# Kernel tuning notes

Hardware: AMD Instinct MI355X
Metric: run time of the kernel (lower is better)

## Reference

```python
import jax, jax.numpy as jnp
import numpy as np

T, B, D, H, NQ = 512, 128, 512, 64, 64  # seq_len, batch, input_dim, hidden_dim == n_qubits
EPS = 1e-5

def setup_inputs() -> dict:
    key = jax.random.key(0)
    ks = jax.random.split(key, 11)
    s = 0.05
    return {
        "inputs": jax.random.normal(ks[0], (T, B, D), jnp.float32),
        "W0": jax.random.normal(ks[1], (4, NQ, D + H), jnp.float32) * s,
        "b0": jax.random.normal(ks[2], (4, NQ), jnp.float32) * s,
        "th0": jax.random.normal(ks[3], (4, NQ), jnp.float32) * s,
        "g0": jnp.ones((H,), jnp.float32),
        "be0": jnp.zeros((H,), jnp.float32),
        "W1": jax.random.normal(ks[4], (4, NQ, H + H), jnp.float32) * s,
        "b1": jax.random.normal(ks[5], (4, NQ), jnp.float32) * s,
        "th1": jax.random.normal(ks[6], (4, NQ), jnp.float32) * s,
        "g1": jnp.ones((H,), jnp.float32),
        "be1": jnp.zeros((H,), jnp.float32),
    }

def _qlstm_layer(x, W, b, th, gamma, beta):
    # x: [T, B, Din]. Faithful to source: h_prev = c_prev = 0 at EVERY timestep
    # (the torch code never writes back `states` inside the time loop), so all
    # timesteps are independent and fully vectorized.
    zeros_h = jnp.zeros(x.shape[:-1] + (H,), x.dtype)
    combined = jnp.concatenate([x, zeros_h], axis=-1)           # [T,B,Din+H]
    # 4 gate linears stacked on leading axis g: forget, input, update, output
    z = jnp.einsum('tbk,gnk->gtbn', combined, W) + b[:, None, None, :]
    # quantum circuit closed form: RX(z_i+th_i) per qubit + CNOT ladder + <Z_k>
    #   => cumprod_{i<=k} cos(z_i + th_i)
    q = jnp.cumprod(jnp.cos(z + th[:, None, None, :]), axis=-1)  # [4,T,B,NQ]
    sg = jax.nn.sigmoid(q)
    i_g = sg[1]
    g_g = jnp.tanh(sg[2])
    o_g = sg[3]
    # c = f * c_prev + i * g, with c_prev == 0  (f gate has no effect)
    c = i_g * g_g                                                # [T,B,H]
    h = o_g * jnp.tanh(c)
    mu = jnp.mean(h, axis=-1, keepdims=True)
    var = jnp.mean((h - mu) ** 2, axis=-1, keepdims=True)
    h_ln = (h - mu) * jax.lax.rsqrt(var + EPS) * gamma + beta
    return h_ln, c

def reference(inputs, W0, b0, th0, g0, be0, W1, b1, th1, g1, be1):
    h0, c0 = _qlstm_layer(inputs, W0, b0, th0, g0, be0)  # layer 0 (no dropout: p=0)
    h1, c1 = _qlstm_layer(h0, W1, b1, th1, g1, be1)      # layer 1
    outputs = h1                                          # [T,B,H]
    # new_states = states at the last timestep: [(h_ln, c)] per layer
    return (outputs, h0[-1], c0[-1], h1[-1], c1[-1])
```

## Files before the change

kernel.cpp:

```cpp
#include <hip/hip_runtime.h>
#include <hip/hip_bf16.h>

typedef __attribute__((ext_vector_type(8))) short bf16x8;
typedef _Float16 f16x8 __attribute__((ext_vector_type(8)));
typedef __attribute__((ext_vector_type(4))) float f32x4;

#define T_SEQ   512
#define B_BATCH 128
#define H_DIM   64
#define MB      64
#define AS_STRIDE 72
#define ZS_STRIDE 193
#define HS_STRIDE 68
#define LASTROW ((T_SEQ - 1) * B_BATCH)

#define W0HF 0
#define W0HB 98304
#define W0LB 196608
#define W1HF 294912
#define W1HB 307200
#define W1LB 319488

__device__ __forceinline__ void splitH(float f, unsigned& hf, unsigned& hb, unsigned& lb) {
    _Float16 h = (_Float16)f;
    hf = (unsigned)__builtin_bit_cast(unsigned short, h);
    float r = f - (float)h;
    hb = (unsigned)__builtin_bit_cast(unsigned short, __float2bfloat16(f));
    lb = (unsigned)__builtin_bit_cast(unsigned short, __float2bfloat16(r));
}

__device__ __forceinline__ void splitH8(const float* p, uint4& Pf, uint4& Pb, uint4& Pl) {
    float4 a = *(const float4*)p;
    float4 b = *(const float4*)(p + 4);
    float v[8] = {a.x, a.y, a.z, a.w, b.x, b.y, b.z, b.w};
    unsigned f[8], hb[8], lb[8];
#pragma unroll
    for (int i = 0; i < 8; ++i) splitH(v[i], f[i], hb[i], lb[i]);
    Pf = (uint4){f[0] | (f[1] << 16), f[2] | (f[3] << 16), f[4] | (f[5] << 16), f[6] | (f[7] << 16)};
    Pb = (uint4){hb[0] | (hb[1] << 16), hb[2] | (hb[3] << 16), hb[4] | (hb[5] << 16), hb[6] | (hb[7] << 16)};
    Pl = (uint4){lb[0] | (lb[1] << 16), lb[2] | (lb[3] << 16), lb[4] | (lb[5] << 16), lb[6] | (lb[7] << 16)};
}

__device__ __forceinline__ f32x4 mfma3(f16x8 af, bf16x8 ab, bf16x8 al,
                                       f16x8 bf, bf16x8 bb, bf16x8 bl, f32x4 c) {
    c = __builtin_amdgcn_mfma_f32_16x16x32_f16(af, bf, c, 0, 0, 0);
    c = __builtin_amdgcn_mfma_f32_16x16x32_bf16(ab, bl, c, 0, 0, 0);
    c = __builtin_amdgcn_mfma_f32_16x16x32_bf16(al, bb, c, 0, 0, 0);
    return c;
}

__device__ __forceinline__ float acc_sigmoid(float x) {
    float e = expf(-x);
    float d = 1.0f + e;
    float r = __builtin_amdgcn_rcpf(d);
    r = r * (2.0f - d * r);
    return r;
}

__device__ __forceinline__ float scan_prod(float v, int lane) {
    for (int d = 1; d < 64; d <<= 1) {
        float t = __shfl_up(v, d);
        v *= (lane >= d) ? t : 1.0f;
    }
    return v;
}

__device__ __forceinline__ float wave_sum(float v) {
    for (int d = 1; d < 64; d <<= 1) v += __shfl_xor(v, d);
    return v;
}

__global__ __launch_bounds__(256) void presplit_w(const float* __restrict__ W0,
                                                  const float* __restrict__ W1,
                                                  unsigned short* __restrict__ ws) {
    int i = blockIdx.x * 256 + threadIdx.x;
    if (i < 98304) {
        int r = i >> 9, k = i & 511;
        unsigned hf, hb, lb;
        splitH(W0[(r + 64) * 576 + k], hf, hb, lb);
        ws[W0HF + i] = (unsigned short)hf;
        ws[W0HB + i] = (unsigned short)hb;
        ws[W0LB + i] = (unsigned short)lb;
    } else if (i < 110592) {
        int j = i - 98304;
        int r = j >> 6, k = j & 63;
        unsigned hf, hb, lb;
        splitH(W1[(r + 64) * 128 + k], hf, hb, lb);
        ws[W1HF + j] = (unsigned short)hf;
        ws[W1HB + j] = (unsigned short)hb;
        ws[W1LB + j] = (unsigned short)lb;
    }
}

__global__ __launch_bounds__(256) void qlstm_fused(
    const float* __restrict__ x,
    const float* __restrict__ b0,
    const float* __restrict__ th0,
    const float* __restrict__ g0,
    const float* __restrict__ be0,
    const float* __restrict__ b1,
    const float* __restrict__ th1,
    const float* __restrict__ g1,
    const float* __restrict__ be1,
    const unsigned short* __restrict__ wsp,
    float* __restrict__ out)
{
    __shared__ __align__(16) char lds[45056];
    unsigned short* phf = (unsigned short*)lds;
    unsigned short* phb = phf + MB * AS_STRIDE;
    unsigned short* plb = phb + MB * AS_STRIDE;
    float* zs = (float*)lds;
    float* hs = (float*)(lds + 27648);

    const int tid = threadIdx.x;
    const long rowbase = (long)blockIdx.x * MB;

    float* out0 = out;
    float* out1 = out + (long)T_SEQ * B_BATCH * H_DIM;
    float* out2 = out1 + B_BATCH * H_DIM;
    float* out3 = out2 + B_BATCH * H_DIM;
    float* out4 = out3 + B_BATCH * H_DIM;

    const int lane = tid & 63;
    const int wave = tid >> 6;
    const int ln   = lane & 15;
    const int quad = lane >> 4;
    const int cw   = wave * 48;

    const float bt0a = b0[64  + lane] + th0[64  + lane];
    const float bt0b = b0[128 + lane] + th0[128 + lane];
    const float bt0c = b0[192 + lane] + th0[192 + lane];
    const float bt1a = b1[64  + lane] + th1[64  + lane];
    const float bt1b = b1[128 + lane] + th1[128 + lane];
    const float bt1c = b1[192 + lane] + th1[192 + lane];
    const float g0v = g0[lane], be0v = be0[lane];
    const float g1v = g1[lane], be1v = be1[lane];

    int brow0[3], brow1[3];
    for (int nt = 0; nt < 3; ++nt) {
        int gc = cw + nt * 16 + ln;
        brow0[nt] = gc * 512;
        brow1[nt] = gc * 64;
    }

    f32x4 acc[4][3];
    for (int mt = 0; mt < 4; ++mt)
        for (int nt = 0; nt < 3; ++nt)
            acc[mt][nt] = (f32x4){0.f, 0.f, 0.f, 0.f};

    for (int kc = 0; kc < 512; kc += 64) {
        for (int it = 0; it < 2; ++it) {
            int e  = it * 256 + tid;
            int r  = e >> 3;
            int k8 = (e & 7) << 3;
            uint4 Pf, Pb, Pl;
            splitH8(x + (rowbase + r) * 512 + kc + k8, Pf, Pb, Pl);
            int ao = r * AS_STRIDE + k8;
            *(uint4*)(phf + ao) = Pf;
            *(uint4*)(phb + ao) = Pb;
            *(uint4*)(plb + ao) = Pl;
        }
        __syncthreads();
        for (int k0 = 0; k0 < 64; k0 += 32) {
            int ka = k0 + quad * 8;
            f16x8  Af[4];
            bf16x8 Ab[4], Al[4];
            for (int mt = 0; mt < 4; ++mt) {
                int ao = (mt * 16 + ln) * AS_STRIDE + ka;
                Af[mt] = *(const f16x8*)(phf + ao);
                Ab[mt] = *(const bf16x8*)(phb + ao);
                Al[mt] = *(const bf16x8*)(plb + ao);
            }
            for (int nt = 0; nt < 3; ++nt) {
                int bo = brow0[nt] + kc + ka;
                f16x8  Bf = *(const f16x8*)(wsp + W0HF + bo);
                bf16x8 Bb = *(const bf16x8*)(wsp + W0HB + bo);
                bf16x8 Bl = *(const bf16x8*)(wsp + W0LB + bo);
                for (int mt = 0; mt < 4; ++mt)
                    acc[mt][nt] = mfma3(Af[mt], Ab[mt], Al[mt], Bf, Bb, Bl, acc[mt][nt]);
            }
        }
        __syncthreads();
    }

    for (int h = 0; h < 2; ++h) {
        for (int mt2 = 0; mt2 < 2; ++mt2) {
            int mt = h * 2 + mt2;
            for (int nt = 0; nt < 3; ++nt)
                for (int i = 0; i < 4; ++i) {
                    int rowl = mt2 * 16 + quad * 4 + i;
                    int col  = cw + nt * 16 + ln;
                    zs[rowl * ZS_STRIDE + col] = acc[mt][nt][i];
                }
        }
        __syncthreads();
        for (int p = 0; p < 8; ++p) {
            int rowl = wave * 8 + p;
            const float* zr = zs + rowl * ZS_STRIDE;
            float c1 = cosf(zr[lane]        + bt0a);
            float c2 = cosf(zr[64  + lane]  + bt0b);
            float c3 = cosf(zr[128 + lane]  + bt0c);
            float q1 = scan_prod(c1, lane);
            float q2 = scan_prod(c2, lane);
            float q3 = scan_prod(c3, lane);
            float ig = acc_sigmoid(q1);
            float gg = tanhf(acc_sigmoid(q2));
            float og = acc_sigmoid(q3);
            float c  = ig * gg;
            float hv = og * tanhf(c);
            float mu = wave_sum(hv) * (1.0f / 64.0f);
            float d  = hv - mu;
            float var = wave_sum(d * d) * (1.0f / 64.0f);
            float rs  = rsqrtf(var + 1e-5f);
            float hl  = d * rs * g0v + be0v;
            int row = h * 32 + rowl;
            hs[row * HS_STRIDE + lane] = hl;
            long tbrow = rowbase + row;
            if (tbrow >= LASTROW) {
                int bidx = (int)(tbrow - LASTROW);
                out1[bidx * 64 + lane] = hl;
                out2[bidx * 64 + lane] = c;
            }
        }
        __syncthreads();
    }

    f32x4 acc2[4][3];
    for (int mt = 0; mt < 4; ++mt)
        for (int nt = 0; nt < 3; ++nt)
            acc2[mt][nt] = (f32x4){0.f, 0.f, 0.f, 0.f};
    for (int k0 = 0; k0 < 64; k0 += 32) {
        int ka = k0 + quad * 8;
        f16x8  Af[4];
        bf16x8 Ab[4], Al[4];
        for (int mt = 0; mt < 4; ++mt) {
            uint4 Pf, Pb, Pl;
            splitH8(hs + (mt * 16 + ln) * HS_STRIDE + ka, Pf, Pb, Pl);
            Af[mt] = __builtin_bit_cast(f16x8, Pf);
            Ab[mt] = __builtin_bit_cast(bf16x8, Pb);
            Al[mt] = __builtin_bit_cast(bf16x8, Pl);
        }
        for (int nt = 0; nt < 3; ++nt) {
            int bo = brow1[nt] + ka;
            f16x8  Bf = *(const f16x8*)(wsp + W1HF + bo);
            bf16x8 Bb = *(const bf16x8*)(wsp + W1HB + bo);
            bf16x8 Bl = *(const bf16x8*)(wsp + W1LB + bo);
            for (int mt = 0; mt < 4; ++mt)
                acc2[mt][nt] = mfma3(Af[mt], Ab[mt], Al[mt], Bf, Bb, Bl, acc2[mt][nt]);
        }
    }

    for (int h = 0; h < 2; ++h) {
        for (int mt2 = 0; mt2 < 2; ++mt2) {
            int mt = h * 2 + mt2;
            for (int nt = 0; nt < 3; ++nt)
                for (int i = 0; i < 4; ++i) {
                    int rowl = mt2 * 16 + quad * 4 + i;
                    int col  = cw + nt * 16 + ln;
                    zs[rowl * ZS_STRIDE + col] = acc2[mt][nt][i];
                }
        }
        __syncthreads();
        for (int p = 0; p < 8; ++p) {
            int rowl = wave * 8 + p;
            const float* zr = zs + rowl * ZS_STRIDE;
            float c1 = cosf(zr[lane]        + bt1a);
            float c2 = cosf(zr[64  + lane]  + bt1b);
            float c3 = cosf(zr[128 + lane]  + bt1c);
            float q1 = scan_prod(c1, lane);
            float q2 = scan_prod(c2, lane);
            float q3 = scan_prod(c3, lane);
            float ig = acc_sigmoid(q1);
            float gg = tanhf(acc_sigmoid(q2));
            float og = acc_sigmoid(q3);
            float c  = ig * gg;
            float hv = og * tanhf(c);
            float mu = wave_sum(hv) * (1.0f / 64.0f);
            float d  = hv - mu;
            float var = wave_sum(d * d) * (1.0f / 64.0f);
            float rs  = rsqrtf(var + 1e-5f);
            float hl  = d * rs * g1v + be1v;
            int row = h * 32 + rowl;
            long tbrow = rowbase + row;
            out0[tbrow * 64 + lane] = hl;
            if (tbrow >= LASTROW) {
                int bidx = (int)(tbrow - LASTROW);
                out3[bidx * 64 + lane] = hl;
                out4[bidx * 64 + lane] = c;
            }
        }
        if (h == 0) __syncthreads();
    }
}

extern "C" void kernel_launch(void* const* d_in, const int* in_sizes, int n_in,
                              void* d_out, int out_size, void* d_ws, size_t ws_size,
                              hipStream_t stream) {
    const float* x   = (const float*)d_in[0];
    const float* W0  = (const float*)d_in[1];
    const float* b0  = (const float*)d_in[2];
    const float* th0 = (const float*)d_in[3];
    const float* g0  = (const float*)d_in[4];
    const float* be0 = (const float*)d_in[5];
    const float* W1  = (const float*)d_in[6];
    const float* b1  = (const float*)d_in[7];
    const float* th1 = (const float*)d_in[8];
    const float* g1  = (const float*)d_in[9];
    const float* be1 = (const float*)d_in[10];
    unsigned short* wsp = (unsigned short*)d_ws;

    presplit_w<<<dim3(432), dim3(256), 0, stream>>>(W0, W1, wsp);
    qlstm_fused<<<dim3(1024), dim3(256), 0, stream>>>(
        x, b0, th0, g0, be0, b1, th1, g1, be1, wsp, (float*)d_out);
}
```

Measured before the change: 358.8 us.

## Make each wave own 16 rows end-to-end, dropping shared A tiles and block barriers

Each wave now computes all 192 gate columns for its own 16 rows. It loads and splits x straight from global into registers instead of staging through shared memory. Only small per-wave scratch buffers are kept, which removes all __syncthreads and shrinks LDS so that launch_bounds can request 4 blocks per SM. In exchange every wave reloads the full weight tile from global/L2 with no reuse across waves, and the epilogue stages results through per-wave LDS one quad at a time.

```diff
diff --git a/kernel.cpp b/kernel.cpp
--- a/kernel.cpp
+++ b/kernel.cpp
@@ -7,10 +7,8 @@
 
 #define T_SEQ   512
 #define B_BATCH 128
-#define H_DIM   64
 #define MB      64
-#define AS_STRIDE 72
-#define ZS_STRIDE 193
+#define ZSL_STRIDE 193
 #define HS_STRIDE 68
 #define LASTROW ((T_SEQ - 1) * B_BATCH)
 
@@ -92,7 +90,7 @@
     }
 }
 
-__global__ __launch_bounds__(256) void qlstm_fused(
+__global__ __launch_bounds__(256, 4) void qlstm_fused(
     const float* __restrict__ x,
     const float* __restrict__ b0,
     const float* __restrict__ th0,
@@ -105,27 +103,24 @@
     const unsigned short* __restrict__ wsp,
     float* __restrict__ out)
 {
-    __shared__ __align__(16) char lds[45056];
-    unsigned short* phf = (unsigned short*)lds;
-    unsigned short* phb = phf + MB * AS_STRIDE;
-    unsigned short* plb = phb + MB * AS_STRIDE;
-    float* zs = (float*)lds;
-    float* hs = (float*)(lds + 27648);
-
-    const int tid = threadIdx.x;
-    const long rowbase = (long)blockIdx.x * MB;
-
-    float* out0 = out;
-    float* out1 = out + (long)T_SEQ * B_BATCH * H_DIM;
-    float* out2 = out1 + B_BATCH * H_DIM;
-    float* out3 = out2 + B_BATCH * H_DIM;
-    float* out4 = out3 + B_BATCH * H_DIM;
-
+    __shared__ __align__(16) char lds[29760];
+
+    const int tid  = threadIdx.x;
     const int lane = tid & 63;
     const int wave = tid >> 6;
     const int ln   = lane & 15;
     const int quad = lane >> 4;
-    const int cw   = wave * 48;
+
+    float* zsl = (float*)lds + wave * (4 * ZSL_STRIDE);
+    float* hsl = (float*)(lds + 12352) + wave * (16 * HS_STRIDE);
+
+    const long rowbase = (long)blockIdx.x * MB + wave * 16;
+
+    float* out0 = out;
+    float* out1 = out + (long)T_SEQ * B_BATCH * 64;
+    float* out2 = out1 + B_BATCH * 64;
+    float* out3 = out2 + B_BATCH * 64;
+    float* out4 = out3 + B_BATCH * 64;
 
     const float bt0a = b0[64  + lane] + th0[64  + lane];
     const float bt0b = b0[128 + lane] + th0[128 + lane];
@@ -136,70 +131,43 @@
     const float g0v = g0[lane], be0v = be0[lane];
     const float g1v = g1[lane], be1v = be1[lane];
 
-    int brow0[3], brow1[3];
-    for (int nt = 0; nt < 3; ++nt) {
-        int gc = cw + nt * 16 + ln;
-        brow0[nt] = gc * 512;
-        brow1[nt] = gc * 64;
-    }
-
-    f32x4 acc[4][3];
-    for (int mt = 0; mt < 4; ++mt)
-        for (int nt = 0; nt < 3; ++nt)
-            acc[mt][nt] = (f32x4){0.f, 0.f, 0.f, 0.f};
-
-    for (int kc = 0; kc < 512; kc += 64) {
-        for (int it = 0; it < 2; ++it) {
-            int e  = it * 256 + tid;
-            int r  = e >> 3;
-            int k8 = (e & 7) << 3;
-            uint4 Pf, Pb, Pl;
-            splitH8(x + (rowbase + r) * 512 + kc + k8, Pf, Pb, Pl);
-            int ao = r * AS_STRIDE + k8;
-            *(uint4*)(phf + ao) = Pf;
-            *(uint4*)(phb + ao) = Pb;
-            *(uint4*)(plb + ao) = Pl;
-        }
-        __syncthreads();
-        for (int k0 = 0; k0 < 64; k0 += 32) {
-            int ka = k0 + quad * 8;
-            f16x8  Af[4];
-            bf16x8 Ab[4], Al[4];
-            for (int mt = 0; mt < 4; ++mt) {
-                int ao = (mt * 16 + ln) * AS_STRIDE + ka;
-                Af[mt] = *(const f16x8*)(phf + ao);
-                Ab[mt] = *(const bf16x8*)(phb + ao);
-                Al[mt] = *(const bf16x8*)(plb + ao);
-            }
-            for (int nt = 0; nt < 3; ++nt) {
-                int bo = brow0[nt] + kc + ka;
-                f16x8  Bf = *(const f16x8*)(wsp + W0HF + bo);
-                bf16x8 Bb = *(const bf16x8*)(wsp + W0HB + bo);
-                bf16x8 Bl = *(const bf16x8*)(wsp + W0LB + bo);
-                for (int mt = 0; mt < 4; ++mt)
-                    acc[mt][nt] = mfma3(Af[mt], Ab[mt], Al[mt], Bf, Bb, Bl, acc[mt][nt]);
-            }
-        }
-        __syncthreads();
-    }
-
-    for (int h = 0; h < 2; ++h) {
-        for (int mt2 = 0; mt2 < 2; ++mt2) {
-            int mt = h * 2 + mt2;
-            for (int nt = 0; nt < 3; ++nt)
-                for (int i = 0; i < 4; ++i) {
-                    int rowl = mt2 * 16 + quad * 4 + i;
-                    int col  = cw + nt * 16 + ln;
-                    zs[rowl * ZS_STRIDE + col] = acc[mt][nt][i];
-                }
-        }
-        __syncthreads();
-        for (int p = 0; p < 8; ++p) {
-            int rowl = wave * 8 + p;
-            const float* zr = zs + rowl * ZS_STRIDE;
-            float c1 = cosf(zr[lane]        + bt0a);
-            float c2 = cosf(zr[64  + lane]  + bt0b);
-            float c3 = cosf(zr[128 + lane]  + bt0c);
+    f32x4 acc[12];
+#pragma unroll
+    for (int nt = 0; nt < 12; ++nt) acc[nt] = (f32x4){0.f, 0.f, 0.f, 0.f};
+
+    const float* xr = x + (rowbase + ln) * 512 + quad * 8;
+    for (int kc = 0; kc < 512; kc += 32) {
+        uint4 Pf, Pb, Pl;
+        splitH8(xr + kc, Pf, Pb, Pl);
+        f16x8  Af = __builtin_bit_cast(f16x8, Pf);
+        bf16x8 Ab = __builtin_bit_cast(bf16x8, Pb);
+        bf16x8 Al = __builtin_bit_cast(bf16x8, Pl);
+        int kb = kc + quad * 8;
+#pragma unroll
+        for (int nt = 0; nt < 12; ++nt) {
+            int bo = (nt * 16 + ln) * 512 + kb;
+            f16x8  Bf = *(const f16x8*)(wsp + W0HF + bo);
+            bf16x8 Bb = *(const bf16x8*)(wsp + W0HB + bo);
+            bf16x8 Bl = *(const bf16x8*)(wsp + W0LB + bo);
+            acc[nt] = mfma3(Af, Ab, Al, Bf, Bb, Bl, acc[nt]);
+        }
+    }
+
+    for (int g2 = 0; g2 < 4; ++g2) {
+        if (quad == g2) {
+#pragma unroll
+            for (int nt = 0; nt < 12; ++nt)
+#pragma unroll
+                for (int i = 0; i < 4; ++i)
+                    zsl[i * ZSL_STRIDE + nt * 16 + ln] = acc[nt][i];
+        }
+        asm volatile("s_waitcnt lgkmcnt(0)" ::: "memory");
+#pragma unroll
+        for (int p = 0; p < 4; ++p) {
+            const float* zr = zsl + p * ZSL_STRIDE;
+            float c1 = cosf(zr[lane]       + bt0a);
+            float c2 = cosf(zr[64 + lane]  + bt0b);
+            float c3 = cosf(zr[128 + lane] + bt0c);
             float q1 = scan_prod(c1, lane);
             float q2 = scan_prod(c2, lane);
             float q3 = scan_prod(c3, lane);
@@ -213,8 +181,8 @@
             float var = wave_sum(d * d) * (1.0f / 64.0f);
             float rs  = rsqrtf(var + 1e-5f);
             float hl  = d * rs * g0v + be0v;
-            int row = h * 32 + rowl;
-            hs[row * HS_STRIDE + lane] = hl;
+            int row = g2 * 4 + p;
+            hsl[row * HS_STRIDE + lane] = hl;
             long tbrow = rowbase + row;
             if (tbrow >= LASTROW) {
                 int bidx = (int)(tbrow - LASTROW);
@@ -222,51 +190,44 @@
                 out2[bidx * 64 + lane] = c;
             }
         }
-        __syncthreads();
-    }
-
-    f32x4 acc2[4][3];
-    for (int mt = 0; mt < 4; ++mt)
-        for (int nt = 0; nt < 3; ++nt)
-            acc2[mt][nt] = (f32x4){0.f, 0.f, 0.f, 0.f};
+    }
+    asm volatile("s_waitcnt lgkmcnt(0)" ::: "memory");
+
+    f32x4 acc2[12];
+#pragma unroll
+    for (int nt = 0; nt < 12; ++nt) acc2[nt] = (f32x4){0.f, 0.f, 0.f, 0.f};
     for (int k0 = 0; k0 < 64; k0 += 32) {
         int ka = k0 + quad * 8;
-        f16x8  Af[4];
-        bf16x8 Ab[4], Al[4];
-        for (int mt = 0; mt < 4; ++mt) {
-            uint4 Pf, Pb, Pl;
-            splitH8(hs + (mt * 16 + ln) * HS_STRIDE + ka, Pf, Pb, Pl);
-            Af[mt] = __builtin_bit_cast(f16x8, Pf);
-            Ab[mt] = __builtin_bit_cast(bf16x8, Pb);
-            Al[mt] = __builtin_bit_cast(bf16x8, Pl);
-        }
-        for (int nt = 0; nt < 3; ++nt) {
-            int bo = brow1[nt] + ka;
+        uint4 Pf, Pb, Pl;
+        splitH8(hsl + ln * HS_STRIDE + ka, Pf, Pb, Pl);
+        f16x8  Af = __builtin_bit_cast(f16x8, Pf);
+        bf16x8 Ab = __builtin_bit_cast(bf16x8, Pb);
+        bf16x8 Al = __builtin_bit_cast(bf16x8, Pl);
+#pragma unroll
+        for (int nt = 0; nt < 12; ++nt) {
+            int bo = (nt * 16 + ln) * 64 + ka;
             f16x8  Bf = *(const f16x8*)(wsp + W1HF + bo);
             bf16x8 Bb = *(const bf16x8*)(wsp + W1HB + bo);
             bf16x8 Bl = *(const bf16x8*)(wsp + W1LB + bo);
-            for (int mt = 0; mt < 4; ++mt)
-                acc2[mt][nt] = mfma3(Af[mt], Ab[mt], Al[mt], Bf, Bb, Bl, acc2[mt][nt]);
-        }
-    }
-
-    for (int h = 0; h < 2; ++h) {
-        for (int mt2 = 0; mt2 < 2; ++mt2) {
-            int mt = h * 2 + mt2;
-            for (int nt = 0; nt < 3; ++nt)
-                for (int i = 0; i < 4; ++i) {
-                    int rowl = mt2 * 16 + quad * 4 + i;
-                    int col  = cw + nt * 16 + ln;
-                    zs[rowl * ZS_STRIDE + col] = acc2[mt][nt][i];
-                }
-        }
-        __syncthreads();
-        for (int p = 0; p < 8; ++p) {
-            int rowl = wave * 8 + p;
-            const float* zr = zs + rowl * ZS_STRIDE;
-            float c1 = cosf(zr[lane]        + bt1a);
-            float c2 = cosf(zr[64  + lane]  + bt1b);
-            float c3 = cosf(zr[128 + lane]  + bt1c);
+            acc2[nt] = mfma3(Af, Ab, Al, Bf, Bb, Bl, acc2[nt]);
+        }
+    }
+
+    for (int g2 = 0; g2 < 4; ++g2) {
+        if (quad == g2) {
+#pragma unroll
+            for (int nt = 0; nt < 12; ++nt)
+#pragma unroll
+                for (int i = 0; i < 4; ++i)
+                    zsl[i * ZSL_STRIDE + nt * 16 + ln] = acc2[nt][i];
+        }
+        asm volatile("s_waitcnt lgkmcnt(0)" ::: "memory");
+#pragma unroll
+        for (int p = 0; p < 4; ++p) {
+            const float* zr = zsl + p * ZSL_STRIDE;
+            float c1 = cosf(zr[lane]       + bt1a);
+            float c2 = cosf(zr[64 + lane]  + bt1b);
+            float c3 = cosf(zr[128 + lane] + bt1c);
             float q1 = scan_prod(c1, lane);
             float q2 = scan_prod(c2, lane);
             float q3 = scan_prod(c3, lane);
@@ -280,7 +241,7 @@
             float var = wave_sum(d * d) * (1.0f / 64.0f);
             float rs  = rsqrtf(var + 1e-5f);
             float hl  = d * rs * g1v + be1v;
-            int row = h * 32 + rowl;
+            int row = g2 * 4 + p;
             long tbrow = rowbase + row;
             out0[tbrow * 64 + lane] = hl;
             if (tbrow >= LASTROW) {
@@ -289,7 +250,6 @@
                 out4[bidx * 64 + lane] = c;
             }
         }
-        if (h == 0) __syncthreads();
     }
 }
 
```

New measurement: 520.5 us. 1.45x slower.
